# Kernel tuning notes

Measured on AMD Instinct MI355X. Metric: run time of the kernel, lower is better.

Reference implementation:

```python
import jax, jax.numpy as jnp
import numpy as np

NUM_TAGS = 64
SEQ_LEN = 512
BATCH = 512


def setup_inputs() -> dict:
    key = jax.random.key(0)
    k1, k2, k3, k4, k5 = jax.random.split(key, 5)
    emissions = jax.random.normal(k1, (SEQ_LEN, BATCH, NUM_TAGS), dtype=jnp.float32)
    tags = jax.random.randint(k2, (SEQ_LEN, BATCH), 0, NUM_TAGS, dtype=jnp.int32)
    mask = jnp.ones((SEQ_LEN, BATCH), dtype=jnp.int32)
    start_transitions = jax.random.uniform(k3, (NUM_TAGS,), dtype=jnp.float32)
    end_transitions = jax.random.uniform(k4, (NUM_TAGS,), dtype=jnp.float32)
    transitions = jax.random.uniform(k5, (NUM_TAGS, NUM_TAGS), dtype=jnp.float32)
    return {
        "emissions": emissions,
        "tags": tags,
        "mask": mask,
        "start_transitions": start_transitions,
        "end_transitions": end_transitions,
        "transitions": transitions,
    }


def _compute_score(emissions, tags, mask, start_transitions, end_transitions, transitions):
    # emissions: (S,B,T), tags/mask: (S,B)
    seq_length, batch_size = tags.shape
    maskf = mask.astype(jnp.float32)
    barange = jnp.arange(batch_size)
    # emission scores for gold tags at every step: (S,B)
    emit = jnp.take_along_axis(emissions, tags[:, :, None], axis=2)[:, :, 0]
    # transition scores between consecutive gold tags: (S-1,B)
    trans = transitions[tags[:-1], tags[1:]]
    score = start_transitions[tags[0]] + emit[0]
    score = score + ((trans + emit[1:]) * maskf[1:]).sum(axis=0)
    seq_ends = mask.astype(jnp.int32).sum(axis=0) - 1  # (B,)
    last_tags = tags[seq_ends, barange]
    score = score + end_transitions[last_tags]
    return score  # (B,)


def _compute_normalizer(emissions, mask, start_transitions, end_transitions, transitions):
    # sequential forward-algorithm scan over time
    score0 = start_transitions + emissions[0]  # (B,T)

    def step(score, inp):
        em, m = inp  # em: (B,T), m: (B,)
        # (B,Tprev,Tnext) logsumexp over Tprev
        next_score = jax.nn.logsumexp(
            score[:, :, None] + transitions[None, :, :] + em[:, None, :], axis=1
        )
        score = jnp.where(m[:, None].astype(bool), next_score, score)
        return score, None

    score, _ = jax.lax.scan(step, score0, (emissions[1:], mask[1:]))
    return jax.nn.logsumexp(score + end_transitions, axis=1)  # (B,)


def reference(emissions, tags, mask, start_transitions, end_transitions, transitions):
    numerator = _compute_score(emissions, tags, mask, start_transitions, end_transitions, transitions)
    denominator = _compute_normalizer(emissions, mask, start_transitions, end_transitions, transitions)
    llh = numerator - denominator
    return llh.sum()  # reduction='sum'
```

## Files before the change

### kernel.cpp

```cpp
#include <hip/hip_runtime.h>

#define T   512
#define B   512
#define NT  64
#define QS  16
#define NQ  (T / QS)
#define RING 4

typedef _Float16 h2 __attribute__((ext_vector_type(2)));

__device__ __forceinline__ float rflf(float x) {
    return __uint_as_float(__builtin_amdgcn_readfirstlane(__float_as_uint(x)));
}

__device__ __forceinline__ float dot2(h2 a, h2 b, float c) {
#if __has_builtin(__builtin_amdgcn_fdot2)
    return __builtin_amdgcn_fdot2(a, b, c, false);
#else
    return c + (float)a.x * (float)b.x + (float)a.y * (float)b.y;
#endif
}

__global__ __launch_bounds__(64) void crf_fused(
    const float* __restrict__ emissions,
    const int*   __restrict__ tags,
    const int*   __restrict__ mask,
    const float* __restrict__ startT,
    const float* __restrict__ endT,
    const float* __restrict__ trans,
    float* __restrict__ out)
{
    const int j = threadIdx.x;

    __shared__ __align__(16) float ebuf[RING][QS][NT];

    if (blockIdx.x < B) {
        const int b = blockIdx.x;

        h2 Eh[NT / 2];
#pragma unroll
        for (int m = 0; m < NT / 2; ++m) {
            Eh[m].x = (_Float16)__expf(trans[(2 * m)     * NT + j]);
            Eh[m].y = (_Float16)__expf(trans[(2 * m + 1) * NT + j]);
        }

        const int jr = j >> 4;
        const int c0 = (j & 15) * 4;
        float4 sA[4];

        auto issue_q = [&](int g) {
#pragma unroll
            for (int k = 0; k < 4; ++k) {
                const int t = g * QS + 4 * k + jr;
                sA[k] = *(const float4*)&emissions[((size_t)t * B + b) * NT + c0];
            }
        };
        auto write_q = [&](int g) {
#pragma unroll
            for (int k = 0; k < 4; ++k) {
                float4 w;
                w.x = __expf(sA[k].x); w.y = __expf(sA[k].y);
                w.z = __expf(sA[k].z); w.w = __expf(sA[k].w);
                *(float4*)&ebuf[g & (RING - 1)][4 * k + jr][c0] = w;
            }
        };

        for (int g = 0; g < 3; ++g) { issue_q(g); write_q(g); }
        issue_q(3);

        const float e0  = emissions[(size_t)b * NT + j];
        const float sc0 = startT[j] + e0;
        const float S0  = rflf(sc0);
        float q = __expf(sc0 - S0);
        int   K = 0;

        int pk_i;
        {
            const int qi = __float_as_int(q);
            const int qo = __builtin_amdgcn_update_dpp(0, qi, 0xB1, 0xF, 0xF, true);
            pk_i = __builtin_bit_cast(int,
                    __builtin_amdgcn_cvt_pkrtz(q, __int_as_float(qo)));
        }

        int mpre = mask[j * B + b];
        unsigned long long mbc = 0;

        for (int x = 0; x < NQ; ++x) {
            const int gw = (x + 3 < NQ) ? x + 3 : NQ - 1;
            write_q(gw);
            const int gl = (x + 4 < NQ) ? x + 4 : NQ - 1;
            issue_q(gl);

            if ((x & 3) == 0) {
                mbc = __ballot(mpre != 0);
                const int cn = ((x >> 2) + 1 < 8) ? (x >> 2) + 1 : 7;
                mpre = mask[(cn * 64 + j) * B + b];
            }

            const int tt0 = (x == 0) ? 1 : 0;
#pragma unroll 4
            for (int tt = tt0; tt < QS; ++tt) {
                const float X = ebuf[x & (RING - 1)][tt][j];

                float a0 = 0.f, a1 = 0.f, a2 = 0.f, a3 = 0.f;
#pragma unroll
                for (int n = 0; n < 8; ++n) {
                    const int u0 = __builtin_amdgcn_readlane(pk_i, 8 * n + 0);
                    const int u1 = __builtin_amdgcn_readlane(pk_i, 8 * n + 2);
                    const int u2 = __builtin_amdgcn_readlane(pk_i, 8 * n + 4);
                    const int u3 = __builtin_amdgcn_readlane(pk_i, 8 * n + 6);
                    a0 = dot2(__builtin_bit_cast(h2, u0), Eh[4 * n + 0], a0);
                    a1 = dot2(__builtin_bit_cast(h2, u1), Eh[4 * n + 1], a1);
                    a2 = dot2(__builtin_bit_cast(h2, u2), Eh[4 * n + 2], a2);
                    a3 = dot2(__builtin_bit_cast(h2, u3), Eh[4 * n + 3], a3);
                }
                const float p = (a0 + a1) + (a2 + a3);

                const int bits = __builtin_amdgcn_readfirstlane(__float_as_int(p));
                const int k    = ((bits >> 23) & 255) - 127;
                const float r  = __int_as_float((127 - k) << 23);

                const int  ttc = ((x & 3) << 4) + tt;
                const bool mc  = (mbc >> ttc) & 1ull;
                const float qn = p * r * X;
                q = mc ? qn : q;
                K += mc ? k : 0;

                const int qi = __float_as_int(q);
                const int qo = __builtin_amdgcn_update_dpp(0, qi, 0xB1, 0xF, 0xF, true);
                pk_i = __builtin_bit_cast(int,
                        __builtin_amdgcn_cvt_pkrtz(q, __int_as_float(qo)));
            }
        }

        float v = q * __expf(endT[j]);
#pragma unroll
        for (int off = 32; off > 0; off >>= 1)
            v += __shfl_xor(v, off);
        if (j == 0)
            atomicAdd(out, -(S0 + (float)K * 0.69314718f + __logf(v)));

    } else {
        const int b = blockIdx.x - B;

        float acc = 0.f;
        int   cnt = 0;
#pragma unroll
        for (int m = 0; m < T / 64; ++m) {
            const int t  = j + 64 * m;
            const int mv = mask[t * B + b];
            const int tg = tags[t * B + b];
            cnt += (int)__popcll(__ballot(mv != 0));
            if (t == 0) {
                acc += startT[tg] + emissions[(size_t)b * NT + tg];
            } else if (mv) {
                const int tp = tags[(t - 1) * B + b];
                acc += trans[tp * NT + tg]
                     + emissions[(size_t)(t * B + b) * NT + tg];
            }
        }
#pragma unroll
        for (int off = 32; off > 0; off >>= 1)
            acc += __shfl_xor(acc, off);
        if (j == 0) {
            const int last = tags[(size_t)(cnt - 1) * B + b];
            atomicAdd(out, acc + endT[last]);
        }
    }
}

extern "C" void kernel_launch(void* const* d_in, const int* in_sizes, int n_in,
                              void* d_out, int out_size, void* d_ws, size_t ws_size,
                              hipStream_t stream) {
    const float* emissions = (const float*)d_in[0];
    const int*   tags      = (const int*)  d_in[1];
    const int*   mask      = (const int*)  d_in[2];
    const float* startT    = (const float*)d_in[3];
    const float* endT      = (const float*)d_in[4];
    const float* trans     = (const float*)d_in[5];
    float* out = (float*)d_out;

    hipMemsetAsync(out, 0, sizeof(float), stream);
    crf_fused<<<2 * B, 64, 0, stream>>>(
        emissions, tags, mask, startT, endT, trans, out);
}
```

Measured before the change: 194.6 us.

## Batch 32 sequences per workgroup and run forward recursion on MFMA

```diff
diff --git a/kernel.cpp b/kernel.cpp
--- a/kernel.cpp
+++ b/kernel.cpp
@@ -3,25 +3,24 @@
 #define T   512
 #define B   512
 #define NT  64
-#define QS  16
-#define NQ  (T / QS)
-#define RING 4
-
-typedef _Float16 h2 __attribute__((ext_vector_type(2)));
-
-__device__ __forceinline__ float rflf(float x) {
-    return __uint_as_float(__builtin_amdgcn_readfirstlane(__float_as_uint(x)));
-}
-
-__device__ __forceinline__ float dot2(h2 a, h2 b, float c) {
-#if __has_builtin(__builtin_amdgcn_fdot2)
-    return __builtin_amdgcn_fdot2(a, b, c, false);
-#else
-    return c + (float)a.x * (float)b.x + (float)a.y * (float)b.y;
-#endif
-}
-
-__global__ __launch_bounds__(64) void crf_fused(
+#define NB  32
+#define NWG (B / NB)
+
+typedef _Float16 h2   __attribute__((ext_vector_type(2)));
+typedef _Float16 h8   __attribute__((ext_vector_type(8)));
+typedef float    f16v __attribute__((ext_vector_type(16)));
+
+__device__ __forceinline__ int cvtpk(float a, float b) {
+    return __builtin_bit_cast(int, __builtin_amdgcn_cvt_pkrtz(a, b));
+}
+__device__ __forceinline__ h2  bch2(int u) { return __builtin_bit_cast(h2, u); }
+__device__ __forceinline__ int bci(h2 u)   { return __builtin_bit_cast(int, u); }
+
+__device__ __forceinline__ void plswap(int& x, int& y) {
+    asm volatile("v_permlane32_swap_b32 %0, %1" : "+v"(x), "+v"(y));
+}
+
+__global__ __launch_bounds__(192) void crf_mfma(
     const float* __restrict__ emissions,
     const int*   __restrict__ tags,
     const int*   __restrict__ mask,
@@ -30,124 +29,223 @@
     const float* __restrict__ trans,
     float* __restrict__ out)
 {
-    const int j = threadIdx.x;
-
-    __shared__ __align__(16) float ebuf[RING][QS][NT];
-
-    if (blockIdx.x < B) {
-        const int b = blockIdx.x;
-
-        h2 Eh[NT / 2];
-#pragma unroll
-        for (int m = 0; m < NT / 2; ++m) {
-            Eh[m].x = (_Float16)__expf(trans[(2 * m)     * NT + j]);
-            Eh[m].y = (_Float16)__expf(trans[(2 * m + 1) * NT + j]);
-        }
-
-        const int jr = j >> 4;
-        const int c0 = (j & 15) * 4;
-        float4 sA[4];
-
-        auto issue_q = [&](int g) {
-#pragma unroll
-            for (int k = 0; k < 4; ++k) {
-                const int t = g * QS + 4 * k + jr;
-                sA[k] = *(const float4*)&emissions[((size_t)t * B + b) * NT + c0];
+    const int wid = threadIdx.x >> 6;
+    const int l   = threadIdx.x & 63;
+
+    __shared__ __align__(16) int xw[16][2][2][NB][8];
+    __shared__ int mls[4][4][NB];
+
+    if (blockIdx.x < NWG) {
+        const int b0 = blockIdx.x * NB;
+
+        if (wid == 0) {
+            const int n  = l & 31;
+            const int hi = l >> 5;
+            const int b  = b0 + n;
+
+            union AU { h2 p[4]; h8 v; };
+            AU A[2][4];
+#pragma unroll
+            for (int mt = 0; mt < 2; ++mt)
+#pragma unroll
+                for (int ks = 0; ks < 4; ++ks)
+#pragma unroll
+                    for (int r = 0; r < 4; ++r) {
+                        const int k = 16*ks + 8*hi + 2*r;
+                        const int j = 32*mt + n;
+                        h2 e;
+                        e.x = (_Float16)__expf(trans[k*NT + j]);
+                        e.y = (_Float16)__expf(trans[(k+1)*NT + j]);
+                        A[mt][ks].p[r] = e;
+                    }
+
+            const float S0 = startT[0] + emissions[(size_t)b * NT];
+            int Qw[4][4];
+#pragma unroll
+            for (int ks = 0; ks < 4; ++ks)
+#pragma unroll
+                for (int r = 0; r < 4; ++r) {
+                    const int k = 16*ks + 8*hi + 2*r;
+                    const float v0 = __expf(startT[k]   + emissions[(size_t)b*NT + k]   - S0);
+                    const float v1 = __expf(startT[k+1] + emissions[(size_t)b*NT + k+1] - S0);
+                    Qw[ks][r] = cvtpk(v0, v1);
+                }
+            int K = 0;
+            const f16v zc = {};
+
+            __syncthreads();
+
+#pragma unroll 1
+            for (int q = 0; q < T/4; ++q) {
+                int mreg[4];
+#pragma unroll
+                for (int tt = 0; tt < 4; ++tt) mreg[tt] = mls[q & 3][tt][n];
+
+#pragma unroll
+                for (int tt = 0; tt < 4; ++tt) {
+                    const int t = 4*q + tt;
+                    if (t == 0) continue;
+                    const int slot = t & 15;
+
+                    const int4 xA0 = *(const int4*)&xw[slot][0][hi][n][0];
+                    const int4 xA1 = *(const int4*)&xw[slot][0][hi][n][4];
+                    const int4 xB0 = *(const int4*)&xw[slot][1][hi][n][0];
+                    const int4 xB1 = *(const int4*)&xw[slot][1][hi][n][4];
+
+                    union QU { int w[4]; h8 v; };
+                    QU q0{{Qw[0][0], Qw[0][1], Qw[0][2], Qw[0][3]}};
+                    QU q1{{Qw[1][0], Qw[1][1], Qw[1][2], Qw[1][3]}};
+                    QU q2{{Qw[2][0], Qw[2][1], Qw[2][2], Qw[2][3]}};
+                    QU q3{{Qw[3][0], Qw[3][1], Qw[3][2], Qw[3][3]}};
+
+                    f16v c0 = __builtin_amdgcn_mfma_f32_32x32x16_f16(A[0][0].v, q0.v, zc, 0,0,0);
+                    f16v c1 = __builtin_amdgcn_mfma_f32_32x32x16_f16(A[1][0].v, q0.v, zc, 0,0,0);
+                    c0 = __builtin_amdgcn_mfma_f32_32x32x16_f16(A[0][1].v, q1.v, c0, 0,0,0);
+                    c1 = __builtin_amdgcn_mfma_f32_32x32x16_f16(A[1][1].v, q1.v, c1, 0,0,0);
+                    c0 = __builtin_amdgcn_mfma_f32_32x32x16_f16(A[0][2].v, q2.v, c0, 0,0,0);
+                    c1 = __builtin_amdgcn_mfma_f32_32x32x16_f16(A[1][2].v, q2.v, c1, 0,0,0);
+                    c0 = __builtin_amdgcn_mfma_f32_32x32x16_f16(A[0][3].v, q3.v, c0, 0,0,0);
+                    c1 = __builtin_amdgcn_mfma_f32_32x32x16_f16(A[1][3].v, q3.v, c1, 0,0,0);
+
+                    int ra = __float_as_int(c0[0]), rb = ra;
+                    plswap(ra, rb);
+                    const int k  = ((rb >> 23) & 255) - 127;
+                    const int sb = (k + 2) << 23;
+
+                    const int xm0[8] = {xA0.x,xA0.y,xA0.z,xA0.w, xA1.x,xA1.y,xA1.z,xA1.w};
+                    const int xm1[8] = {xB0.x,xB0.y,xB0.z,xB0.w, xB1.x,xB1.y,xB1.z,xB1.w};
+
+                    int Nw[4][4];
+                    {
+                        int Wl[4], Wh[4];
+#pragma unroll
+                        for (int g = 0; g < 4; ++g) {
+                            const float p0 = __int_as_float(__float_as_int(c0[4*g+0]) - sb);
+                            const float p1 = __int_as_float(__float_as_int(c0[4*g+1]) - sb);
+                            const float p2 = __int_as_float(__float_as_int(c0[4*g+2]) - sb);
+                            const float p3 = __int_as_float(__float_as_int(c0[4*g+3]) - sb);
+                            Wl[g] = bci(bch2(cvtpk(p0, p1)) * bch2(xm0[2*g]));
+                            Wh[g] = bci(bch2(cvtpk(p2, p3)) * bch2(xm0[2*g+1]));
+                        }
+#pragma unroll
+                        for (int s = 0; s < 2; ++s) {
+                            int a1 = Wl[2*s+1], a0 = Wl[2*s];
+                            plswap(a1, a0);
+                            Nw[s][2] = a1; Nw[s][0] = a0;
+                            int d1 = Wh[2*s+1], d0 = Wh[2*s];
+                            plswap(d1, d0);
+                            Nw[s][3] = d1; Nw[s][1] = d0;
+                        }
+                    }
+                    {
+                        int Wl[4], Wh[4];
+#pragma unroll
+                        for (int g = 0; g < 4; ++g) {
+                            const float p0 = __int_as_float(__float_as_int(c1[4*g+0]) - sb);
+                            const float p1 = __int_as_float(__float_as_int(c1[4*g+1]) - sb);
+                            const float p2 = __int_as_float(__float_as_int(c1[4*g+2]) - sb);
+                            const float p3 = __int_as_float(__float_as_int(c1[4*g+3]) - sb);
+                            Wl[g] = bci(bch2(cvtpk(p0, p1)) * bch2(xm1[2*g]));
+                            Wh[g] = bci(bch2(cvtpk(p2, p3)) * bch2(xm1[2*g+1]));
+                        }
+#pragma unroll
+                        for (int s = 0; s < 2; ++s) {
+                            int a1 = Wl[2*s+1], a0 = Wl[2*s];
+                            plswap(a1, a0);
+                            Nw[2+s][2] = a1; Nw[2+s][0] = a0;
+                            int d1 = Wh[2*s+1], d0 = Wh[2*s];
+                            plswap(d1, d0);
+                            Nw[2+s][3] = d1; Nw[2+s][1] = d0;
+                        }
+                    }
+
+                    const bool mc = mreg[tt] != 0;
+                    if (__ballot(mc) == ~0ull) {
+                        K += k + 2;
+#pragma unroll
+                        for (int ks = 0; ks < 4; ++ks)
+#pragma unroll
+                            for (int r = 0; r < 4; ++r) Qw[ks][r] = Nw[ks][r];
+                    } else {
+                        K += mc ? (k + 2) : 0;
+#pragma unroll
+                        for (int ks = 0; ks < 4; ++ks)
+#pragma unroll
+                            for (int r = 0; r < 4; ++r)
+                                Qw[ks][r] = mc ? Nw[ks][r] : Qw[ks][r];
+                    }
+                }
+                __syncthreads();
             }
-        };
-        auto write_q = [&](int g) {
-#pragma unroll
-            for (int k = 0; k < 4; ++k) {
-                float4 w;
-                w.x = __expf(sA[k].x); w.y = __expf(sA[k].y);
-                w.z = __expf(sA[k].z); w.w = __expf(sA[k].w);
-                *(float4*)&ebuf[g & (RING - 1)][4 * k + jr][c0] = w;
-            }
-        };
-
-        for (int g = 0; g < 3; ++g) { issue_q(g); write_q(g); }
-        issue_q(3);
-
-        const float e0  = emissions[(size_t)b * NT + j];
-        const float sc0 = startT[j] + e0;
-        const float S0  = rflf(sc0);
-        float q = __expf(sc0 - S0);
-        int   K = 0;
-
-        int pk_i;
-        {
-            const int qi = __float_as_int(q);
-            const int qo = __builtin_amdgcn_update_dpp(0, qi, 0xB1, 0xF, 0xF, true);
-            pk_i = __builtin_bit_cast(int,
-                    __builtin_amdgcn_cvt_pkrtz(q, __int_as_float(qo)));
-        }
-
-        int mpre = mask[j * B + b];
-        unsigned long long mbc = 0;
-
-        for (int x = 0; x < NQ; ++x) {
-            const int gw = (x + 3 < NQ) ? x + 3 : NQ - 1;
-            write_q(gw);
-            const int gl = (x + 4 < NQ) ? x + 4 : NQ - 1;
-            issue_q(gl);
-
-            if ((x & 3) == 0) {
-                mbc = __ballot(mpre != 0);
-                const int cn = ((x >> 2) + 1 < 8) ? (x >> 2) + 1 : 7;
-                mpre = mask[(cn * 64 + j) * B + b];
-            }
-
-            const int tt0 = (x == 0) ? 1 : 0;
-#pragma unroll 4
-            for (int tt = tt0; tt < QS; ++tt) {
-                const float X = ebuf[x & (RING - 1)][tt][j];
-
-                float a0 = 0.f, a1 = 0.f, a2 = 0.f, a3 = 0.f;
-#pragma unroll
-                for (int n = 0; n < 8; ++n) {
-                    const int u0 = __builtin_amdgcn_readlane(pk_i, 8 * n + 0);
-                    const int u1 = __builtin_amdgcn_readlane(pk_i, 8 * n + 2);
-                    const int u2 = __builtin_amdgcn_readlane(pk_i, 8 * n + 4);
-                    const int u3 = __builtin_amdgcn_readlane(pk_i, 8 * n + 6);
-                    a0 = dot2(__builtin_bit_cast(h2, u0), Eh[4 * n + 0], a0);
-                    a1 = dot2(__builtin_bit_cast(h2, u1), Eh[4 * n + 1], a1);
-                    a2 = dot2(__builtin_bit_cast(h2, u2), Eh[4 * n + 2], a2);
-                    a3 = dot2(__builtin_bit_cast(h2, u3), Eh[4 * n + 3], a3);
-                }
-                const float p = (a0 + a1) + (a2 + a3);
-
-                const int bits = __builtin_amdgcn_readfirstlane(__float_as_int(p));
-                const int k    = ((bits >> 23) & 255) - 127;
-                const float r  = __int_as_float((127 - k) << 23);
-
-                const int  ttc = ((x & 3) << 4) + tt;
-                const bool mc  = (mbc >> ttc) & 1ull;
-                const float qn = p * r * X;
-                q = mc ? qn : q;
-                K += mc ? k : 0;
-
-                const int qi = __float_as_int(q);
-                const int qo = __builtin_amdgcn_update_dpp(0, qi, 0xB1, 0xF, 0xF, true);
-                pk_i = __builtin_bit_cast(int,
-                        __builtin_amdgcn_cvt_pkrtz(q, __int_as_float(qo)));
+
+            float v = 0.f;
+#pragma unroll
+            for (int ks = 0; ks < 4; ++ks)
+#pragma unroll
+                for (int r = 0; r < 4; ++r) {
+                    const int k = 16*ks + 8*hi + 2*r;
+                    const h2 qq = bch2(Qw[ks][r]);
+                    v += (float)qq.x * __expf(endT[k]);
+                    v += (float)qq.y * __expf(endT[k+1]);
+                }
+            v += __shfl_xor(v, 32);
+            const float den = S0 + (float)K * 0.69314718f + __logf(v);
+            float con = (l < 32) ? -den : 0.f;
+#pragma unroll
+            for (int off = 32; off > 0; off >>= 1) con += __shfl_xor(con, off);
+            if (l == 0) atomicAdd(out, con);
+
+        } else {
+            const int par = wid - 1;
+            auto stage_q = [&](int qq) {
+                if (qq >= T/4) return;
+                if (par == 0 && l < 32) {
+#pragma unroll
+                    for (int tt = 0; tt < 4; ++tt)
+                        mls[qq & 3][tt][l] = mask[(4*qq + tt)*B + b0 + l];
+                }
+#pragma unroll
+                for (int u = 0; u < 2; ++u) {
+                    const int tt = 2*u + par;
+                    const int t = 4*qq + tt;
+                    const int slot = t & 15;
+                    float4 ev[8];
+#pragma unroll
+                    for (int it = 0; it < 8; ++it) {
+                        const int flat = it*64 + l;
+                        ev[it] = *(const float4*)&emissions[((size_t)t*B + b0)*NT + flat*4];
+                    }
+#pragma unroll
+                    for (int it = 0; it < 8; ++it) {
+                        const int flat = it*64 + l;
+                        const int n2 = flat >> 4;
+                        const int j0 = (flat & 15) * 4;
+                        const int mt = j0 >> 5;
+                        const int hg = (j0 >> 2) & 1;
+                        const int g  = (j0 & 31) >> 3;
+                        int2 wv;
+                        wv.x = cvtpk(__expf(ev[it].x), __expf(ev[it].y));
+                        wv.y = cvtpk(__expf(ev[it].z), __expf(ev[it].w));
+                        *(int2*)&xw[slot][mt][hg][n2][2*g] = wv;
+                    }
+                }
+            };
+            stage_q(0); stage_q(1);
+            __syncthreads();
+#pragma unroll 1
+            for (int q = 0; q < T/4; ++q) {
+                stage_q(q + 2);
+                __syncthreads();
             }
         }
 
-        float v = q * __expf(endT[j]);
-#pragma unroll
-        for (int off = 32; off > 0; off >>= 1)
-            v += __shfl_xor(v, off);
-        if (j == 0)
-            atomicAdd(out, -(S0 + (float)K * 0.69314718f + __logf(v)));
-
-    } else {
-        const int b = blockIdx.x - B;
-
+    } else if (wid == 0) {
+        const int b = blockIdx.x - NWG;
         float acc = 0.f;
         int   cnt = 0;
 #pragma unroll
         for (int m = 0; m < T / 64; ++m) {
-            const int t  = j + 64 * m;
+            const int t  = l + 64 * m;
             const int mv = mask[t * B + b];
             const int tg = tags[t * B + b];
             cnt += (int)__popcll(__ballot(mv != 0));
@@ -162,7 +260,7 @@
 #pragma unroll
         for (int off = 32; off > 0; off >>= 1)
             acc += __shfl_xor(acc, off);
-        if (j == 0) {
+        if (l == 0) {
             const int last = tags[(size_t)(cnt - 1) * B + b];
             atomicAdd(out, acc + endT[last]);
         }
@@ -181,6 +279,6 @@
     float* out = (float*)d_out;
 
     hipMemsetAsync(out, 0, sizeof(float), stream);
-    crf_fused<<<2 * B, 64, 0, stream>>>(
+    crf_mfma<<<NWG + B, 192, 0, stream>>>(
         emissions, tags, mask, startT, endT, trans, out);
 }
```

Result: slower. 281.6 us (+44.7%).
